# Optimization experiments

Measured on AMD Instinct MI355X. Metric: run time of the kernel, lower is better.

## Reference

```python
import jax, jax.numpy as jnp
import numpy as np

B, S, H, NH = 8, 512, 768, 12
HD = H // NH  # 64


def setup_inputs() -> dict:
    key = jax.random.key(0)
    ks = jax.random.split(key, 8)
    scale = 0.02
    return {
        "hidden_states": jax.random.normal(ks[0], (B, S, H), dtype=jnp.float32),
        "attention_mask": jnp.zeros((B, 1, 1, S), dtype=jnp.float32),
        "Wq": jax.random.normal(ks[1], (H, H), dtype=jnp.float32) * scale,
        "bq": jnp.zeros((H,), dtype=jnp.float32),
        "Wk": jax.random.normal(ks[2], (H, H), dtype=jnp.float32) * scale,
        "bk": jnp.zeros((H,), dtype=jnp.float32),
        "Wv": jax.random.normal(ks[3], (H, H), dtype=jnp.float32) * scale,
        "bv": jnp.zeros((H,), dtype=jnp.float32),
    }


def reference(hidden_states, attention_mask, Wq, bq, Wk, bk, Wv, bv):
    # BERT-style self-attention (dropout disabled / eval mode).
    def heads(x):  # [B,S,H] -> [B,NH,S,HD]
        return x.reshape(B, S, NH, HD).transpose(0, 2, 1, 3)

    q = heads(hidden_states @ Wq.T + bq)
    k = heads(hidden_states @ Wk.T + bk)
    v = heads(hidden_states @ Wv.T + bv)

    scores = jnp.einsum("bnqd,bnkd->bnqk", q, k) / jnp.sqrt(jnp.float32(HD))
    scores = scores + attention_mask  # additive mask broadcast over heads/queries
    probs = jax.nn.softmax(scores, axis=-1)
    ctx = jnp.einsum("bnqk,bnkd->bnqd", probs, v)
    return ctx.transpose(0, 2, 1, 3).reshape(B, S, H)
```

## Files before the change

### kernel.cpp

```cpp
#include <hip/hip_runtime.h>
#include <hip/hip_bf16.h>

typedef __bf16 bf16x8 __attribute__((ext_vector_type(8)));
typedef float f32x4 __attribute__((ext_vector_type(4)));
typedef float f32x16 __attribute__((ext_vector_type(16)));
typedef unsigned int u32x2 __attribute__((ext_vector_type(2)));
typedef unsigned int u32x4 __attribute__((ext_vector_type(4)));
typedef unsigned short us8 __attribute__((ext_vector_type(8)));

#define MFMA32(a, b, c) __builtin_amdgcn_mfma_f32_32x32x16_bf16((a), (b), (c), 0, 0, 0)

#define BATCH 8
#define SEQ 512
#define HID 768
#define NHEAD 12
#define HDIM 64

__device__ __forceinline__ unsigned short f2bf(float f) {
    unsigned int u = __float_as_uint(f);
    u += 0x7fffu + ((u >> 16) & 1u);
    return (unsigned short)(u >> 16);
}

__device__ __forceinline__ unsigned int cvtpk_bf16(float lo, float hi) {
    unsigned int r;
    asm("v_cvt_pk_bf16_f32 %0, %1, %2" : "=v"(r) : "v"(lo), "v"(hi));
    return r;
}

__global__ __launch_bounds__(256) void cvt_all_kernel(const float4* __restrict__ hs,
                                                      const float4* __restrict__ Wq,
                                                      const float4* __restrict__ Wk,
                                                      const float4* __restrict__ Wv,
                                                      unsigned short* __restrict__ hsb,
                                                      unsigned short* __restrict__ wb) {
    __shared__ us8 lds[768];

    const int tid = threadIdx.x;
    const int id = blockIdx.x;
    const int T = id >> 2;
    const int q = id & 3;

    const float4* src;
    int row0;
    unsigned short* dst;
    int Tout;
    if (T < 128) {
        src = hs; row0 = T * 32; dst = hsb; Tout = T;
    } else {
        int tw = T - 128;
        int which = tw / 24;
        src = (which == 0) ? Wq : ((which == 1) ? Wk : Wv);
        row0 = (tw - which * 24) * 32;
        dst = wb; Tout = tw;
    }

#pragma unroll
    for (int it = 0; it < 3; ++it) {
        int g = it * 256 + tid;
        int row = g / 24, ccl = g - row * 24;
        int fidx = (row0 + row) * 192 + (q * 24 + ccl) * 2;
        float4 v0 = src[fidx], v1 = src[fidx + 1];
        us8 o;
        o[0] = f2bf(v0.x); o[1] = f2bf(v0.y); o[2] = f2bf(v0.z); o[3] = f2bf(v0.w);
        o[4] = f2bf(v1.x); o[5] = f2bf(v1.y); o[6] = f2bf(v1.z); o[7] = f2bf(v1.w);
        int cell = row * 24 + ccl;
        lds[cell ^ (row & 7)] = o;
    }
    __syncthreads();

    const int w = tid >> 6, l = tid & 63;
    const int row = l & 31, h5 = l >> 5;
#pragma unroll
    for (int j = 0; j < 3; ++j) {
        int ktl = w * 3 + j;
        int kt = q * 12 + ktl;
        int cell = row * 24 + ktl * 2 + h5;
        us8 o = lds[cell ^ (row & 7)];
        *reinterpret_cast<us8*>(dst + ((size_t)Tout * 48 + kt) * 512 + l * 8) = o;
    }
}

__global__ __launch_bounds__(512, 6) void qkv_gemm_kernel(const unsigned short* __restrict__ hsb,
                                                          const unsigned short* __restrict__ wb,
                                                          const float* __restrict__ bq,
                                                          const float* __restrict__ bk,
                                                          const float* __restrict__ bv,
                                                          unsigned short* __restrict__ Qf,
                                                          unsigned short* __restrict__ Kf,
                                                          unsigned short* __restrict__ VTf) {
    __shared__ __align__(16) char smem[49152];
    float* combine = (float*)smem;
    unsigned short* tb = (unsigned short*)smem;

    const int tid = threadIdx.x;
    const int w = tid >> 6;
    const int l = tid & 63;
    const int lq = l & 31, h5 = l >> 5;
    const int quad = w & 3;
    const int kh = w >> 2;
    const int qm = quad >> 1, qn = quad & 1;

    const int id = blockIdx.x;
    const int xcd = id & 7, j = id >> 3;
    const int tm = (xcd >> 1) * 16 + j / 6;
    const int tn = (xcd & 1) * 6 + j % 6;

    const int fa = tm * 2 + qm;
    const int fb0 = tn * 6 + qn * 3;

    const unsigned short* pa  = hsb + (size_t)fa * 48 * 512 + kh * 24 * 512 + l * 8;
    const unsigned short* pb0 = wb + (size_t)fb0 * 48 * 512 + kh * 24 * 512 + l * 8;
    const unsigned short* pb1 = pb0 + 48 * 512;
    const unsigned short* pb2 = pb1 + 48 * 512;

    f32x16 acc0 = {}, acc1 = {}, acc2 = {};

#pragma unroll 4
    for (int kt = 0; kt < 24; ++kt) {
        bf16x8 a  = *reinterpret_cast<const bf16x8*>(pa + kt * 512);
        bf16x8 b0 = *reinterpret_cast<const bf16x8*>(pb0 + kt * 512);
        bf16x8 b1 = *reinterpret_cast<const bf16x8*>(pb1 + kt * 512);
        bf16x8 b2 = *reinterpret_cast<const bf16x8*>(pb2 + kt * 512);
        acc0 = MFMA32(a, b0, acc0);
        acc1 = MFMA32(a, b1, acc1);
        acc2 = MFMA32(a, b2, acc2);
    }

    f32x16 accs[3] = {acc0, acc1, acc2};

    if (kh == 1) {
#pragma unroll
        for (int ni = 0; ni < 3; ++ni)
#pragma unroll
            for (int r = 0; r < 16; ++r)
                combine[(size_t)quad * 3072 + (ni * 16 + r) * 64 + l] = accs[ni][r];
    }
    __syncthreads();
    if (kh == 0) {
#pragma unroll
        for (int ni = 0; ni < 3; ++ni)
#pragma unroll
            for (int r = 0; r < 16; ++r)
                accs[ni][r] += combine[(size_t)quad * 3072 + (ni * 16 + r) * 64 + l];
    }
    __syncthreads();

    const int which = tn / 4;
    const int b = tm >> 3;

    if (kh == 0) {
#pragma unroll
        for (int ni = 0; ni < 3; ++ni) {
            int d_local = qn * 96 + ni * 32 + lq;
            int col = tn * 192 + d_local;
            int oo = col - which * HID;
            const float* bias = (which == 0) ? bq : ((which == 1) ? bk : bv);
            float bvv = bias[oo];
            float scale = (which == 0) ? 0.125f : 1.0f;
#pragma unroll
            for (int g = 0; g < 4; ++g) {
                int s_base = qm * 32 + 8 * g + 4 * h5;
                if (which == 2) {
                    ushort4 pk;
                    pk.x = f2bf(accs[ni][4 * g + 0] + bvv);
                    pk.y = f2bf(accs[ni][4 * g + 1] + bvv);
                    pk.z = f2bf(accs[ni][4 * g + 2] + bvv);
                    pk.w = f2bf(accs[ni][4 * g + 3] + bvv);
                    int byte = d_local * 128 + ((s_base * 2) ^ ((d_local & 7) << 4));
                    *reinterpret_cast<ushort4*>((char*)tb + byte) = pk;
                } else {
#pragma unroll
                    for (int r2 = 0; r2 < 4; ++r2) {
                        int s_local = s_base + r2;
                        int dbyte = d_local * 2;
                        int byte = s_local * 384 + (dbyte & 0x180)
                                 + ((dbyte ^ ((s_local & 7) << 4)) & 0x7F);
                        *reinterpret_cast<unsigned short*>((char*)tb + byte) =
                            f2bf((accs[ni][4 * g + r2] + bvv) * scale);
                    }
                }
            }
        }
    }
    __syncthreads();

    if (which != 2) {
        unsigned short* dstF = (which == 0) ? Qf : Kf;
        const int tnb = tn - which * 4;
#pragma unroll
        for (int j2 = 0; j2 < 3; ++j2) {
            int fi = w * 3 + j2;
            int dc = fi & 3;
            int t2 = fi >> 2;
            int hl = t2 % 3, qt_l = t2 / 3;
            int head = tnb * 3 + hl;
            int qt = (tm & 7) * 2 + qt_l;
            int s_local = qt_l * 32 + lq;
            int dbyte = (hl * 64 + dc * 16 + h5 * 8) * 2;
            int byte = s_local * 384 + (dbyte & 0x180)
                     + ((dbyte ^ ((s_local & 7) << 4)) & 0x7F);
            us8 v = *reinterpret_cast<const us8*>((char*)tb + byte);
            size_t off = ((((size_t)(b * NHEAD + head)) * 16 + qt) * 4 + dc) * 512 + l * 8;
            *reinterpret_cast<us8*>(dstF + off) = v;
        }
    } else {
#pragma unroll
        for (int j2 = 0; j2 < 3; ++j2) {
            int fi = w * 3 + j2;
            int kt2l = fi & 3;
            int t2 = fi >> 2;
            int hl = t2 % 3, nt = t2 / 3;
            int head = (tn - 8) * 3 + hl;
            int d_local = hl * 64 + nt * 32 + lq;
            int sbyte = kt2l * 32 + h5 * 16;
            int byte = d_local * 128 + (sbyte ^ ((d_local & 7) << 4));
            us8 v = *reinterpret_cast<const us8*>((char*)tb + byte);
            int kt2 = (tm & 7) * 4 + kt2l;
            size_t off = ((((size_t)(b * NHEAD + head)) * 2 + nt) * 32 + kt2) * 512 + l * 8;
            *reinterpret_cast<us8*>(VTf + off) = v;
        }
    }
}

__global__ __launch_bounds__(256, 3) void attn_kernel(const unsigned short* __restrict__ Qf,
                                                      const unsigned short* __restrict__ Kf,
                                                      const unsigned short* __restrict__ VTf,
                                                      const float* __restrict__ mask,
                                                      float* __restrict__ out) {
    __shared__ float lds_ctx[2][32][64];
    __shared__ float lds_den[2][32];

    const int tid = threadIdx.x;
    const int w = tid >> 6;
    const int l = tid & 63;
    const int lq = l & 31;
    const int h5 = l >> 5;
    const int qg = w & 1;
    const int kh = w >> 1;

    const int id = blockIdx.x;
    const int hh = id % 96;
    const int qb = id / 96;
    const int b = hh / 12;
    const int hd = hh % 12;

    const int bh = b * NHEAD + hd;
    const int q0 = qb * 64 + qg * 32;
    const float4* mask4 = (const float4*)mask;

    bf16x8 qf[4];
    {
        const unsigned short* qbase = Qf + (((size_t)bh * 16 + (qb * 2 + qg)) * 4) * 512 + l * 8;
#pragma unroll
        for (int dc = 0; dc < 4; ++dc)
            qf[dc] = *reinterpret_cast<const bf16x8*>(qbase + dc * 512);
    }

    const unsigned short* kbase  = Kf + (((size_t)bh * 16 + kh * 8) * 4) * 512 + l * 8;
    const unsigned short* vbase0 = VTf + (((size_t)bh * 2 + 0) * 32 + kh * 16) * 512 + l * 8;
    const unsigned short* vbase1 = VTf + (((size_t)bh * 2 + 1) * 32 + kh * 16) * 512 + l * 8;

    f32x16 ctx0 = {};
    f32x16 ctx1 = {};
    float den = 0.f;

#pragma unroll
    for (int kb = 0; kb < 8; ++kb) {
        bf16x8 kf[4];
#pragma unroll
        for (int dc = 0; dc < 4; ++dc)
            kf[dc] = *reinterpret_cast<const bf16x8*>(kbase + (kb * 4 + dc) * 512);

        f32x16 T = {};
#pragma unroll
        for (int dc = 0; dc < 4; ++dc)
            T = MFMA32(kf[dc], qf[dc], T);

        bf16x8 vf00 = *reinterpret_cast<const bf16x8*>(vbase0 + kb * 2 * 512);
        bf16x8 vf10 = *reinterpret_cast<const bf16x8*>(vbase0 + (kb * 2 + 1) * 512);
        bf16x8 vf01 = *reinterpret_cast<const bf16x8*>(vbase1 + kb * 2 * 512);
        bf16x8 vf11 = *reinterpret_cast<const bf16x8*>(vbase1 + (kb * 2 + 1) * 512);

        const int k0 = kh * 256 + kb * 32;
        float4 mv[4];
#pragma unroll
        for (int g = 0; g < 4; ++g)
            mv[g] = mask4[b * 128 + (k0 >> 2) + 2 * g + h5];

        float p[16];
#pragma unroll
        for (int r = 0; r < 16; ++r) {
            float mval = (r & 3) == 0 ? mv[r >> 2].x : ((r & 3) == 1 ? mv[r >> 2].y
                       : ((r & 3) == 2 ? mv[r >> 2].z : mv[r >> 2].w));
            p[r] = __expf(T[r] + mval);
            den += p[r];
        }

        bf16x8 pa[2];
#pragma unroll
        for (int c = 0; c < 2; ++c) {
            int base = c * 8;
            unsigned int lo01 = cvtpk_bf16(p[base + 0], p[base + 1]);
            unsigned int lo23 = cvtpk_bf16(p[base + 2], p[base + 3]);
            unsigned int hi01 = cvtpk_bf16(p[base + 4], p[base + 5]);
            unsigned int hi23 = cvtpk_bf16(p[base + 6], p[base + 7]);
            u32x2 s1 = __builtin_amdgcn_permlane32_swap(lo01, hi01, false, false);
            u32x2 s2 = __builtin_amdgcn_permlane32_swap(lo23, hi23, false, false);
            u32x4 words = {s1[0], s2[0], s1[1], s2[1]};
            pa[c] = __builtin_bit_cast(bf16x8, words);
        }

        ctx0 = MFMA32(pa[0], vf00, ctx0);
        ctx0 = MFMA32(pa[1], vf10, ctx0);
        ctx1 = MFMA32(pa[0], vf01, ctx1);
        ctx1 = MFMA32(pa[1], vf11, ctx1);
    }

    float den_full = den + __shfl_xor(den, 32);

    if (kh == 1) {
        if (l < 32) lds_den[qg][l] = den_full;
#pragma unroll
        for (int r = 0; r < 16; ++r) {
            int qr = (r & 3) + 8 * (r >> 2) + 4 * h5;
            lds_ctx[qg][qr][lq] = ctx0[r];
            lds_ctx[qg][qr][32 + lq] = ctx1[r];
        }
    }
    __syncthreads();
    if (kh == 0) {
        float den_tot = den_full + lds_den[qg][lq];
#pragma unroll
        for (int r = 0; r < 16; ++r) {
            int qr = (r & 3) + 8 * (r >> 2) + 4 * h5;
            float dn = 1.0f / __shfl(den_tot, qr);
            size_t rowoff = ((size_t)b * SEQ + q0 + qr) * HID + hd * HDIM;
            out[rowoff + lq]      = (ctx0[r] + lds_ctx[qg][qr][lq]) * dn;
            out[rowoff + 32 + lq] = (ctx1[r] + lds_ctx[qg][qr][32 + lq]) * dn;
        }
    }
}

extern "C" void kernel_launch(void* const* d_in, const int* in_sizes, int n_in,
                              void* d_out, int out_size, void* d_ws, size_t ws_size,
                              hipStream_t stream) {
    const float* hs   = (const float*)d_in[0];
    const float* mask = (const float*)d_in[1];
    const float* Wq   = (const float*)d_in[2];
    const float* bq   = (const float*)d_in[3];
    const float* Wk   = (const float*)d_in[4];
    const float* bk   = (const float*)d_in[5];
    const float* Wv   = (const float*)d_in[6];
    const float* bv   = (const float*)d_in[7];
    float* out = (float*)d_out;

    char* ws = (char*)d_ws;
    unsigned short* hsb = (unsigned short*)(ws);
    unsigned short* wb  = (unsigned short*)(ws + 6291456);
    unsigned short* Qf  = (unsigned short*)(ws + 9830400);
    unsigned short* Kf  = (unsigned short*)(ws + 16121856);
    unsigned short* VTf = (unsigned short*)(ws + 22413312);

    cvt_all_kernel<<<800, 256, 0, stream>>>((const float4*)hs, (const float4*)Wq,
                                            (const float4*)Wk, (const float4*)Wv,
                                            hsb, wb);
    qkv_gemm_kernel<<<768, 512, 0, stream>>>(hsb, wb, bq, bk, bv, Qf, Kf, VTf);
    attn_kernel<<<768, 256, 0, stream>>>(Qf, Kf, VTf, mask, out);
}
```

Measured before the change: 56.26 us.

## Halve QKV GEMM block to 4 waves, each computing a 2x3 MFMA tile

The QKV projection block shrinks from 8 waves to 4, and each wave now computes a 64x96 output tile (2x3 32x32 MFMAs) instead of 32x96. Each loaded B fragment is reused across two A fragments, which cuts global/L2 loads per MFMA and the number of waves doing the split-K combine. The cost is more accumulator registers per wave (6 f32x16) and fewer waves per block to hide load latency. The launch bound no longer specifies a minimum occupancy.

```diff
diff --git a/kernel.cpp b/kernel.cpp
--- a/kernel.cpp
+++ b/kernel.cpp
@@ -81,14 +81,14 @@
     }
 }
 
-__global__ __launch_bounds__(512, 6) void qkv_gemm_kernel(const unsigned short* __restrict__ hsb,
-                                                          const unsigned short* __restrict__ wb,
-                                                          const float* __restrict__ bq,
-                                                          const float* __restrict__ bk,
-                                                          const float* __restrict__ bv,
-                                                          unsigned short* __restrict__ Qf,
-                                                          unsigned short* __restrict__ Kf,
-                                                          unsigned short* __restrict__ VTf) {
+__global__ __launch_bounds__(256) void qkv_gemm_kernel(const unsigned short* __restrict__ hsb,
+                                                       const unsigned short* __restrict__ wb,
+                                                       const float* __restrict__ bq,
+                                                       const float* __restrict__ bk,
+                                                       const float* __restrict__ bv,
+                                                       unsigned short* __restrict__ Qf,
+                                                       unsigned short* __restrict__ Kf,
+                                                       unsigned short* __restrict__ VTf) {
     __shared__ __align__(16) char smem[49152];
     float* combine = (float*)smem;
     unsigned short* tb = (unsigned short*)smem;
@@ -97,52 +97,60 @@
     const int w = tid >> 6;
     const int l = tid & 63;
     const int lq = l & 31, h5 = l >> 5;
-    const int quad = w & 3;
-    const int kh = w >> 2;
-    const int qm = quad >> 1, qn = quad & 1;
+    const int qn = w & 1;
+    const int kh = w >> 1;
 
     const int id = blockIdx.x;
     const int xcd = id & 7, j = id >> 3;
     const int tm = (xcd >> 1) * 16 + j / 6;
     const int tn = (xcd & 1) * 6 + j % 6;
 
-    const int fa = tm * 2 + qm;
+    const int fa0 = tm * 2;
     const int fb0 = tn * 6 + qn * 3;
 
-    const unsigned short* pa  = hsb + (size_t)fa * 48 * 512 + kh * 24 * 512 + l * 8;
+    const unsigned short* paA = hsb + (size_t)fa0 * 48 * 512 + kh * 24 * 512 + l * 8;
+    const unsigned short* paB = paA + 48 * 512;
     const unsigned short* pb0 = wb + (size_t)fb0 * 48 * 512 + kh * 24 * 512 + l * 8;
     const unsigned short* pb1 = pb0 + 48 * 512;
     const unsigned short* pb2 = pb1 + 48 * 512;
 
-    f32x16 acc0 = {}, acc1 = {}, acc2 = {};
-
-#pragma unroll 4
+    f32x16 a00 = {}, a01 = {}, a02 = {}, a10 = {}, a11 = {}, a12 = {};
+
+#pragma unroll 2
     for (int kt = 0; kt < 24; ++kt) {
-        bf16x8 a  = *reinterpret_cast<const bf16x8*>(pa + kt * 512);
+        bf16x8 a0 = *reinterpret_cast<const bf16x8*>(paA + kt * 512);
+        bf16x8 a1 = *reinterpret_cast<const bf16x8*>(paB + kt * 512);
         bf16x8 b0 = *reinterpret_cast<const bf16x8*>(pb0 + kt * 512);
         bf16x8 b1 = *reinterpret_cast<const bf16x8*>(pb1 + kt * 512);
         bf16x8 b2 = *reinterpret_cast<const bf16x8*>(pb2 + kt * 512);
-        acc0 = MFMA32(a, b0, acc0);
-        acc1 = MFMA32(a, b1, acc1);
-        acc2 = MFMA32(a, b2, acc2);
-    }
-
-    f32x16 accs[3] = {acc0, acc1, acc2};
+        a00 = MFMA32(a0, b0, a00);
+        a01 = MFMA32(a0, b1, a01);
+        a02 = MFMA32(a0, b2, a02);
+        a10 = MFMA32(a1, b0, a10);
+        a11 = MFMA32(a1, b1, a11);
+        a12 = MFMA32(a1, b2, a12);
+    }
+
+    f32x16 accs[2][3] = {{a00, a01, a02}, {a10, a11, a12}};
 
     if (kh == 1) {
 #pragma unroll
-        for (int ni = 0; ni < 3; ++ni)
-#pragma unroll
-            for (int r = 0; r < 16; ++r)
-                combine[(size_t)quad * 3072 + (ni * 16 + r) * 64 + l] = accs[ni][r];
+        for (int mi = 0; mi < 2; ++mi)
+#pragma unroll
+            for (int ni = 0; ni < 3; ++ni)
+#pragma unroll
+                for (int r = 0; r < 16; ++r)
+                    combine[((size_t)qn * 96 + (mi * 3 + ni) * 16 + r) * 64 + l] = accs[mi][ni][r];
     }
     __syncthreads();
     if (kh == 0) {
 #pragma unroll
-        for (int ni = 0; ni < 3; ++ni)
-#pragma unroll
-            for (int r = 0; r < 16; ++r)
-                accs[ni][r] += combine[(size_t)quad * 3072 + (ni * 16 + r) * 64 + l];
+        for (int mi = 0; mi < 2; ++mi)
+#pragma unroll
+            for (int ni = 0; ni < 3; ++ni)
+#pragma unroll
+                for (int r = 0; r < 16; ++r)
+                    accs[mi][ni][r] += combine[((size_t)qn * 96 + (mi * 3 + ni) * 16 + r) * 64 + l];
     }
     __syncthreads();
 
@@ -159,25 +167,28 @@
             float bvv = bias[oo];
             float scale = (which == 0) ? 0.125f : 1.0f;
 #pragma unroll
-            for (int g = 0; g < 4; ++g) {
-                int s_base = qm * 32 + 8 * g + 4 * h5;
-                if (which == 2) {
-                    ushort4 pk;
-                    pk.x = f2bf(accs[ni][4 * g + 0] + bvv);
-                    pk.y = f2bf(accs[ni][4 * g + 1] + bvv);
-                    pk.z = f2bf(accs[ni][4 * g + 2] + bvv);
-                    pk.w = f2bf(accs[ni][4 * g + 3] + bvv);
-                    int byte = d_local * 128 + ((s_base * 2) ^ ((d_local & 7) << 4));
-                    *reinterpret_cast<ushort4*>((char*)tb + byte) = pk;
-                } else {
-#pragma unroll
-                    for (int r2 = 0; r2 < 4; ++r2) {
-                        int s_local = s_base + r2;
-                        int dbyte = d_local * 2;
-                        int byte = s_local * 384 + (dbyte & 0x180)
-                                 + ((dbyte ^ ((s_local & 7) << 4)) & 0x7F);
-                        *reinterpret_cast<unsigned short*>((char*)tb + byte) =
-                            f2bf((accs[ni][4 * g + r2] + bvv) * scale);
+            for (int mi = 0; mi < 2; ++mi) {
+#pragma unroll
+                for (int g = 0; g < 4; ++g) {
+                    int s_base = mi * 32 + 8 * g + 4 * h5;
+                    if (which == 2) {
+                        ushort4 pk;
+                        pk.x = f2bf(accs[mi][ni][4 * g + 0] + bvv);
+                        pk.y = f2bf(accs[mi][ni][4 * g + 1] + bvv);
+                        pk.z = f2bf(accs[mi][ni][4 * g + 2] + bvv);
+                        pk.w = f2bf(accs[mi][ni][4 * g + 3] + bvv);
+                        int byte = d_local * 128 + ((s_base * 2) ^ ((d_local & 7) << 4));
+                        *reinterpret_cast<ushort4*>((char*)tb + byte) = pk;
+                    } else {
+#pragma unroll
+                        for (int r2 = 0; r2 < 4; ++r2) {
+                            int s_local = s_base + r2;
+                            int dbyte = d_local * 2;
+                            int byte = s_local * 384 + (dbyte & 0x180)
+                                     + ((dbyte ^ ((s_local & 7) << 4)) & 0x7F);
+                            *reinterpret_cast<unsigned short*>((char*)tb + byte) =
+                                f2bf((accs[mi][ni][4 * g + r2] + bvv) * scale);
+                        }
                     }
                 }
             }
@@ -189,8 +200,8 @@
         unsigned short* dstF = (which == 0) ? Qf : Kf;
         const int tnb = tn - which * 4;
 #pragma unroll
-        for (int j2 = 0; j2 < 3; ++j2) {
-            int fi = w * 3 + j2;
+        for (int j2 = 0; j2 < 6; ++j2) {
+            int fi = w * 6 + j2;
             int dc = fi & 3;
             int t2 = fi >> 2;
             int hl = t2 % 3, qt_l = t2 / 3;
@@ -206,8 +217,8 @@
         }
     } else {
 #pragma unroll
-        for (int j2 = 0; j2 < 3; ++j2) {
-            int fi = w * 3 + j2;
+        for (int j2 = 0; j2 < 6; ++j2) {
+            int fi = w * 6 + j2;
             int kt2l = fi & 3;
             int t2 = fi >> 2;
             int hl = t2 % 3, nt = t2 / 3;
@@ -365,6 +376,6 @@
     cvt_all_kernel<<<800, 256, 0, stream>>>((const float4*)hs, (const float4*)Wq,
                                             (const float4*)Wk, (const float4*)Wv,
                                             hsb, wb);
-    qkv_gemm_kernel<<<768, 512, 0, stream>>>(hsb, wb, bq, bk, bv, Qf, Kf, VTf);
+    qkv_gemm_kernel<<<768, 256, 0, stream>>>(hsb, wb, bq, bk, bv, Qf, Kf, VTf);
     attn_kernel<<<768, 256, 0, stream>>>(Qf, Kf, VTf, mask, out);
 }
```

New measurement: 56.15 us. About the same (-0.2%).
